# Kernel tuning notes

Measured on AMD Instinct MI355X. Metric: run time of the kernel, lower is better.

The kernel has to match this reference:

```python
import jax, jax.numpy as jnp
import numpy as np

BN_EPS = 1e-5


def _gin_layer(x, agg, W1, b1, W2, b2, gamma, beta):
    # GINConv with eps=0: h = MLP(x + sum_{j in N(i)} x_j)
    h = x + agg
    h = jax.nn.relu(h @ W1 + b1)
    h = jax.nn.relu(h @ W2 + b2)
    # BatchNorm1d, training mode (batch statistics, biased variance)
    mean = jnp.mean(h, axis=0)
    var = jnp.var(h, axis=0)
    return (h - mean) * jax.lax.rsqrt(var + BN_EPS) * gamma + beta


def setup_inputs() -> dict:
    key = jax.random.key(0)
    ks = jax.random.split(key, 10)
    N, E, D_IN, D_H, D_OUT = 100000, 1600000, 128, 128, 128
    s = lambda fi, fo: (2.0 / (fi + fo)) ** 0.5
    return {
        "x": jax.random.normal(ks[0], (N, D_IN), dtype=jnp.float32),
        "edge_index": jax.random.randint(ks[1], (2, E), 0, N, dtype=jnp.int64),
        "W1a": jax.random.normal(ks[2], (D_IN, D_H), dtype=jnp.float32) * s(D_IN, D_H),
        "b1a": jnp.zeros((D_H,), jnp.float32),
        "W1b": jax.random.normal(ks[3], (D_H, D_H), dtype=jnp.float32) * s(D_H, D_H),
        "b1b": jnp.zeros((D_H,), jnp.float32),
        "g1": jnp.ones((D_H,), jnp.float32),
        "be1": jnp.zeros((D_H,), jnp.float32),
        "W2a": jax.random.normal(ks[4], (D_H, D_H), dtype=jnp.float32) * s(D_H, D_H),
        "b2a": jnp.zeros((D_H,), jnp.float32),
        "W2b": jax.random.normal(ks[5], (D_H, D_OUT), dtype=jnp.float32) * s(D_H, D_OUT),
        "b2b": jnp.zeros((D_OUT,), jnp.float32),
        "g2": jnp.ones((D_OUT,), jnp.float32),
        "be2": jnp.zeros((D_OUT,), jnp.float32),
    }


def reference(x, edge_index, W1a, b1a, W1b, b1b, g1, be1,
              W2a, b2a, W2b, b2b, g2, be2):
    N = x.shape[0]
    src, dst = edge_index[0], edge_index[1]
    # layer 1: scatter-add neighbor features into targets
    agg = jax.ops.segment_sum(x[src], dst, num_segments=N)
    h = _gin_layer(x, agg, W1a, b1a, W1b, b1b, g1, be1)
    # layer 2
    agg = jax.ops.segment_sum(h[src], dst, num_segments=N)
    h = _gin_layer(h, agg, W2a, b2a, W2b, b2b, g2, be2)
    return h
```

## Files before the change

kernel.cpp:

```cpp
#include <hip/hip_runtime.h>
#include <hip/hip_bf16.h>

typedef unsigned int u32;
typedef unsigned short u16;
typedef short bf16x8 __attribute__((ext_vector_type(8)));
typedef float f32x4 __attribute__((ext_vector_type(4)));

static __device__ __forceinline__ float bf_lo(u32 v) { return __uint_as_float(v << 16); }
static __device__ __forceinline__ float bf_hi(u32 v) { return __uint_as_float(v & 0xffff0000u); }
static __device__ __forceinline__ u16 f2bf(float f) {
    u32 u = __float_as_uint(f);
    u32 r = u + 0x7fffu + ((u >> 16) & 1u);
    return (u16)(r >> 16);
}
static __device__ __forceinline__ u32 pack2(float a, float b) {
    return ((u32)f2bf(b) << 16) | (u32)f2bf(a);
}

__global__ __launch_bounds__(256) void convert_k(const float* __restrict__ in,
                                                 u32* __restrict__ out2, int total4)
{
    for (int i = blockIdx.x * 256 + threadIdx.x; i < total4; i += gridDim.x * 256) {
        float4 v = reinterpret_cast<const float4*>(in)[i];
        out2[2 * i + 0] = pack2(v.x, v.y);
        out2[2 * i + 1] = pack2(v.z, v.w);
    }
}

__global__ __launch_bounds__(256) void wprep_k(const float* __restrict__ Wa,
                                               const float* __restrict__ Wb,
                                               const float* __restrict__ Wc,
                                               const float* __restrict__ Wd,
                                               u16* __restrict__ Wf)
{
    int g = blockIdx.x * 256 + threadIdx.x;
    int which = g >> 14;
    int t = g & 16383;
    const float* W = which == 0 ? Wa : which == 1 ? Wb : which == 2 ? Wc : Wd;
    int j  = t & 7;
    int l  = (t >> 3) & 63;
    int nb = (t >> 9) & 7;
    int kg = (t >> 12) & 3;
    int k  = kg * 32 + (l >> 4) * 8 + j;
    int n  = nb * 16 + (l & 15);
    Wf[g] = f2bf(W[k * 128 + n]);
}

__global__ __launch_bounds__(256) void bhist_k(const int* __restrict__ edst,
                                               int* __restrict__ gcount, int E, int NB)
{
    __shared__ int lh[1024];
    for (int i = threadIdx.x; i < 1024; i += 256) lh[i] = 0;
    __syncthreads();
    for (int e = blockIdx.x * 256 + threadIdx.x; e < E; e += gridDim.x * 256)
        atomicAdd(&lh[edst[e] >> 7], 1);
    __syncthreads();
    for (int b = threadIdx.x; b < NB; b += 256)
        if (lh[b]) atomicAdd(&gcount[b], lh[b]);
}

__global__ __launch_bounds__(1024) void bscan_k(const int* __restrict__ gcount,
                                                int* __restrict__ goffs,
                                                int* __restrict__ gcur, int NB)
{
    __shared__ int s[1024];
    int t = threadIdx.x;
    int v = (t < NB) ? gcount[t] : 0;
    s[t] = v; __syncthreads();
    for (int d = 1; d < 1024; d <<= 1) {
        int x = (t >= d) ? s[t - d] : 0;
        __syncthreads();
        s[t] += x;
        __syncthreads();
    }
    if (t < NB) { int o = s[t] - v; goffs[t] = o; gcur[t] = o; }
    if (t == NB - 1) goffs[NB] = s[t];
}

__global__ __launch_bounds__(256) void bfill_k(const int* __restrict__ esrc,
                                               const int* __restrict__ edst,
                                               int* __restrict__ gcur,
                                               u32* __restrict__ bpacked, int E, int NB)
{
    __shared__ int lh[1024];
    __shared__ int lbase[1024];
    int t = threadIdx.x;
    for (int i = t; i < 1024; i += 256) lh[i] = 0;
    __syncthreads();
    int per = (E + gridDim.x - 1) / gridDim.x;
    int lo = blockIdx.x * per;
    int hi = lo + per; if (hi > E) hi = E;
    for (int e = lo + t; e < hi; e += 256) atomicAdd(&lh[edst[e] >> 7], 1);
    __syncthreads();
    for (int b = t; b < NB; b += 256) {
        int c = lh[b];
        lbase[b] = c ? atomicAdd(&gcur[b], c) : 0;
    }
    __syncthreads();
    for (int i = t; i < 1024; i += 256) lh[i] = 0;
    __syncthreads();
    for (int e = lo + t; e < hi; e += 256) {
        int d = edst[e];
        int b = d >> 7;
        int idx = atomicAdd(&lh[b], 1);
        bpacked[lbase[b] + idx] = ((u32)(d & 127) << 17) | (u32)esrc[e];
    }
}

__global__ __launch_bounds__(256) void fsort_k(const u32* __restrict__ bpacked,
                                               const int* __restrict__ goffs,
                                               int* __restrict__ slots,
                                               int* __restrict__ offs,
                                               int* __restrict__ deg, int N)
{
    __shared__ int cnt[128];
    __shared__ int roff[128];
    __shared__ int sb[128];
    int b = blockIdx.x, t = threadIdx.x;
    int start = goffs[b], end = goffs[b + 1];
    if (t < 128) cnt[t] = 0;
    __syncthreads();
    for (int e = start + t; e < end; e += 256)
        atomicAdd(&cnt[bpacked[e] >> 17], 1);
    __syncthreads();
    if (t < 128) sb[t] = cnt[t];
    __syncthreads();
    for (int d = 1; d < 128; d <<= 1) {
        int x = (t < 128 && t >= d) ? sb[t - d] : 0;
        __syncthreads();
        if (t < 128) sb[t] += x;
        __syncthreads();
    }
    if (t < 128) roff[t] = sb[t] - cnt[t];
    __syncthreads();
    int row0 = b * 128;
    if (t < 128 && row0 + t < N) {
        offs[row0 + t] = start + roff[t];
        deg[row0 + t]  = cnt[t];
    }
    if (t < 128) cnt[t] = 0;
    __syncthreads();
    for (int e = start + t; e < end; e += 256) {
        u32 pk = bpacked[e];
        int local = (int)(pk >> 17);
        int idx = atomicAdd(&cnt[local], 1);
        slots[start + roff[local] + idx] = (int)(pk & 0x1FFFF);
    }
}

#define ROWP(s) reinterpret_cast<const u32*>(xbase + ((size_t)(u32)(s) << 8))

template<int MODE>
__global__ __launch_bounds__(256) void gather_k(const u32* __restrict__ xb2,
                                                const int* __restrict__ offs,
                                                const int* __restrict__ deg,
                                                const int* __restrict__ slots,
                                                const float* __restrict__ stats_in,
                                                const float* __restrict__ g_in,
                                                const float* __restrict__ be_in,
                                                u32* __restrict__ xa2, int N)
{
    __shared__ float sc[128], sh[128];
    int t = threadIdx.x;
    if (MODE == 1) {
        if (t < 128) {
            float invN = 1.0f / (float)N;
            float mean = stats_in[t] * invN;
            float var  = stats_in[128 + t] * invN - mean * mean;
            float s = g_in[t] * rsqrtf(var + 1e-5f);
            sc[t] = s;
            sh[t] = be_in[t] - mean * s;
        }
        __syncthreads();
    }

    int row = blockIdx.x * 4 + (t >> 6);
    if (row >= N) return;
    int lane = t & 63;
    const char* xbase = (const char*)xb2;

    u32 self = ROWP(row)[lane];
    float ax0 = bf_lo(self), ay0 = bf_hi(self);
    float ax1 = 0.f, ay1 = 0.f, ax2 = 0.f, ay2 = 0.f, ax3 = 0.f, ay3 = 0.f;

    int ustart = __builtin_amdgcn_readfirstlane(offs[row]);
    int udg    = __builtin_amdgcn_readfirstlane(deg[row]);

    int e = 0;
    for (; e + 16 <= udg; e += 16) {
        int s0 = slots[ustart + e + 0],  s1 = slots[ustart + e + 1];
        int s2 = slots[ustart + e + 2],  s3 = slots[ustart + e + 3];
        int s4 = slots[ustart + e + 4],  s5 = slots[ustart + e + 5];
        int s6 = slots[ustart + e + 6],  s7 = slots[ustart + e + 7];
        int s8 = slots[ustart + e + 8],  s9 = slots[ustart + e + 9];
        int sA = slots[ustart + e + 10], sB = slots[ustart + e + 11];
        int sC = slots[ustart + e + 12], sD = slots[ustart + e + 13];
        int sE = slots[ustart + e + 14], sF = slots[ustart + e + 15];
        u32 v0 = ROWP(s0)[lane], v1 = ROWP(s1)[lane];
        u32 v2 = ROWP(s2)[lane], v3 = ROWP(s3)[lane];
        u32 v4 = ROWP(s4)[lane], v5 = ROWP(s5)[lane];
        u32 v6 = ROWP(s6)[lane], v7 = ROWP(s7)[lane];
        u32 v8 = ROWP(s8)[lane], v9 = ROWP(s9)[lane];
        u32 vA = ROWP(sA)[lane], vB = ROWP(sB)[lane];
        u32 vC = ROWP(sC)[lane], vD = ROWP(sD)[lane];
        u32 vE = ROWP(sE)[lane], vF = ROWP(sF)[lane];
        ax0 += bf_lo(v0); ay0 += bf_hi(v0);  ax1 += bf_lo(v1); ay1 += bf_hi(v1);
        ax2 += bf_lo(v2); ay2 += bf_hi(v2);  ax3 += bf_lo(v3); ay3 += bf_hi(v3);
        ax0 += bf_lo(v4); ay0 += bf_hi(v4);  ax1 += bf_lo(v5); ay1 += bf_hi(v5);
        ax2 += bf_lo(v6); ay2 += bf_hi(v6);  ax3 += bf_lo(v7); ay3 += bf_hi(v7);
        ax0 += bf_lo(v8); ay0 += bf_hi(v8);  ax1 += bf_lo(v9); ay1 += bf_hi(v9);
        ax2 += bf_lo(vA); ay2 += bf_hi(vA);  ax3 += bf_lo(vB); ay3 += bf_hi(vB);
        ax0 += bf_lo(vC); ay0 += bf_hi(vC);  ax1 += bf_lo(vD); ay1 += bf_hi(vD);
        ax2 += bf_lo(vE); ay2 += bf_hi(vE);  ax3 += bf_lo(vF); ay3 += bf_hi(vF);
    }
    if (e + 8 <= udg) {
        int s0 = slots[ustart + e + 0], s1 = slots[ustart + e + 1];
        int s2 = slots[ustart + e + 2], s3 = slots[ustart + e + 3];
        int s4 = slots[ustart + e + 4], s5 = slots[ustart + e + 5];
        int s6 = slots[ustart + e + 6], s7 = slots[ustart + e + 7];
        u32 v0 = ROWP(s0)[lane], v1 = ROWP(s1)[lane];
        u32 v2 = ROWP(s2)[lane], v3 = ROWP(s3)[lane];
        u32 v4 = ROWP(s4)[lane], v5 = ROWP(s5)[lane];
        u32 v6 = ROWP(s6)[lane], v7 = ROWP(s7)[lane];
        ax0 += bf_lo(v0); ay0 += bf_hi(v0);  ax1 += bf_lo(v1); ay1 += bf_hi(v1);
        ax2 += bf_lo(v2); ay2 += bf_hi(v2);  ax3 += bf_lo(v3); ay3 += bf_hi(v3);
        ax0 += bf_lo(v4); ay0 += bf_hi(v4);  ax1 += bf_lo(v5); ay1 += bf_hi(v5);
        ax2 += bf_lo(v6); ay2 += bf_hi(v6);  ax3 += bf_lo(v7); ay3 += bf_hi(v7);
        e += 8;
    }
    if (e + 4 <= udg) {
        int s0 = slots[ustart + e + 0], s1 = slots[ustart + e + 1];
        int s2 = slots[ustart + e + 2], s3 = slots[ustart + e + 3];
        u32 v0 = ROWP(s0)[lane], v1 = ROWP(s1)[lane];
        u32 v2 = ROWP(s2)[lane], v3 = ROWP(s3)[lane];
        ax0 += bf_lo(v0); ay0 += bf_hi(v0);  ax1 += bf_lo(v1); ay1 += bf_hi(v1);
        ax2 += bf_lo(v2); ay2 += bf_hi(v2);  ax3 += bf_lo(v3); ay3 += bf_hi(v3);
        e += 4;
    }
    for (; e < udg; ++e) {
        int s = slots[ustart + e];
        u32 v = ROWP(s)[lane];
        ax0 += bf_lo(v); ay0 += bf_hi(v);
    }

    float ax = (ax0 + ax1) + (ax2 + ax3);
    float ay = (ay0 + ay1) + (ay2 + ay3);
    if (MODE == 1) {
        float d1 = (float)(udg + 1);
        ax = sc[2 * lane]     * ax + d1 * sh[2 * lane];
        ay = sc[2 * lane + 1] * ay + d1 * sh[2 * lane + 1];
    }
    xa2[(size_t)row * 64 + lane] = pack2(ax, ay);
}

__global__ __launch_bounds__(256) void mlp_mfma_k(
    const u16* __restrict__ xa,
    const u16* __restrict__ wfa, const float* __restrict__ ba,
    const u16* __restrict__ wfb, const float* __restrict__ bb,
    u16* __restrict__ hb_out, float* __restrict__ partial, int N)
{
    __shared__ short ta[64 * 128];
    __shared__ float ssum[256];

    int t = threadIdx.x;
    int w = t >> 6, l = t & 63;
    int row0 = blockIdx.x * 64;

    for (int c = t; c < 1024; c += 256) {
        int r = c >> 4, ci = c & 15;
        int dst = (r * 128 + ci * 8) ^ ((r & 7) << 3);
        f32x4 v;
        if (row0 + r < N)
            v = *reinterpret_cast<const f32x4*>(xa + ((size_t)(row0 + r) * 128 + ci * 8));
        else
            v = f32x4{0.f, 0.f, 0.f, 0.f};
        *reinterpret_cast<f32x4*>(ta + dst) = v;
    }

    bf16x8 wf[2][4];
#pragma unroll
    for (int nr = 0; nr < 2; ++nr) {
        int nb = 2 * w + nr;
#pragma unroll
        for (int kg = 0; kg < 4; ++kg)
            wf[nr][kg] = *reinterpret_cast<const bf16x8*>(
                wfa + ((size_t)((kg * 8 + nb) * 64 + l)) * 8);
    }
    __syncthreads();

    int rr = l & 15;
    int kg8 = l >> 4;

    f32x4 acc[4][2];
#pragma unroll
    for (int mr = 0; mr < 4; ++mr)
#pragma unroll
        for (int nr = 0; nr < 2; ++nr)
            acc[mr][nr] = f32x4{0.f, 0.f, 0.f, 0.f};

#pragma unroll
    for (int mr = 0; mr < 4; ++mr) {
        int r = mr * 16 + rr;
        bf16x8 af[4];
#pragma unroll
        for (int kg = 0; kg < 4; ++kg) {
            int idx = (r * 128 + kg * 32 + kg8 * 8) ^ ((r & 7) << 3);
            af[kg] = *reinterpret_cast<const bf16x8*>(ta + idx);
        }
#pragma unroll
        for (int nr = 0; nr < 2; ++nr)
#pragma unroll
            for (int kg = 0; kg < 4; ++kg)
                acc[mr][nr] = __builtin_amdgcn_mfma_f32_16x16x32_bf16(
                    af[kg], wf[nr][kg], acc[mr][nr], 0, 0, 0);
    }
    __syncthreads();

    int colb = w * 32;
    float b0 = ba[colb + rr];
    float b1 = ba[colb + 16 + rr];
#pragma unroll
    for (int mr = 0; mr < 4; ++mr)
#pragma unroll
        for (int nr = 0; nr < 2; ++nr) {
            float bb_ = nr ? b1 : b0;
            int col = colb + nr * 16 + rr;
#pragma unroll
            for (int reg = 0; reg < 4; ++reg) {
                int row = mr * 16 + kg8 * 4 + reg;
                float v = fmaxf(acc[mr][nr][reg] + bb_, 0.0f);
                ta[(row * 128 + col) ^ ((row & 7) << 3)] = (short)f2bf(v);
            }
        }

#pragma unroll
    for (int nr = 0; nr < 2; ++nr) {
        int nb = 2 * w + nr;
#pragma unroll
        for (int kg = 0; kg < 4; ++kg)
            wf[nr][kg] = *reinterpret_cast<const bf16x8*>(
                wfb + ((size_t)((kg * 8 + nb) * 64 + l)) * 8);
    }
    __syncthreads();

#pragma unroll
    for (int mr = 0; mr < 4; ++mr)
#pragma unroll
        for (int nr = 0; nr < 2; ++nr)
            acc[mr][nr] = f32x4{0.f, 0.f, 0.f, 0.f};

#pragma unroll
    for (int mr = 0; mr < 4; ++mr) {
        int r = mr * 16 + rr;
        bf16x8 af[4];
#pragma unroll
        for (int kg = 0; kg < 4; ++kg) {
            int idx = (r * 128 + kg * 32 + kg8 * 8) ^ ((r & 7) << 3);
            af[kg] = *reinterpret_cast<const bf16x8*>(ta + idx);
        }
#pragma unroll
        for (int nr = 0; nr < 2; ++nr)
#pragma unroll
            for (int kg = 0; kg < 4; ++kg)
                acc[mr][nr] = __builtin_amdgcn_mfma_f32_16x16x32_bf16(
                    af[kg], wf[nr][kg], acc[mr][nr], 0, 0, 0);
    }

    float c0 = bb[colb + rr];
    float c1 = bb[colb + 16 + rr];
    float s0 = 0.f, q0 = 0.f, s1 = 0.f, q1 = 0.f;
#pragma unroll
    for (int mr = 0; mr < 4; ++mr) {
#pragma unroll
        for (int reg = 0; reg < 4; ++reg) {
            int row = row0 + mr * 16 + kg8 * 4 + reg;
            bool ok = row < N;
            float v0 = fmaxf(acc[mr][0][reg] + c0, 0.0f);
            float v1 = fmaxf(acc[mr][1][reg] + c1, 0.0f);
            if (ok) {
                hb_out[(size_t)row * 128 + colb + rr]      = f2bf(v0);
                hb_out[(size_t)row * 128 + colb + 16 + rr] = f2bf(v1);
                s0 += v0; q0 += v0 * v0;
                s1 += v1; q1 += v1 * v1;
            }
        }
    }
    s0 += __shfl_xor(s0, 16); s0 += __shfl_xor(s0, 32);
    q0 += __shfl_xor(q0, 16); q0 += __shfl_xor(q0, 32);
    s1 += __shfl_xor(s1, 16); s1 += __shfl_xor(s1, 32);
    q1 += __shfl_xor(q1, 16); q1 += __shfl_xor(q1, 32);
    if (kg8 == 0) {
        ssum[colb + rr]            = s0;
        ssum[128 + colb + rr]      = q0;
        ssum[colb + 16 + rr]       = s1;
        ssum[128 + colb + 16 + rr] = q1;
    }
    __syncthreads();
    partial[(size_t)blockIdx.x * 256 + t] = ssum[t];
}

__global__ __launch_bounds__(256) void reduce_k(const float* __restrict__ partial,
                                                float* __restrict__ stats, int nrows)
{
    int t = threadIdx.x;
    int chunk = (nrows + gridDim.x - 1) / gridDim.x;
    int lo = blockIdx.x * chunk;
    int hi = lo + chunk; if (hi > nrows) hi = nrows;
    float acc = 0.f;
    for (int r = lo; r < hi; ++r)
        acc += partial[(size_t)r * 256 + t];
    if (hi > lo) atomicAdd(&stats[t], acc);
}

__global__ __launch_bounds__(256) void bn_apply_bf_k(
    const u32* __restrict__ h2b, const float* __restrict__ stats,
    const float* __restrict__ gamma, const float* __restrict__ beta,
    float* __restrict__ out, int N)
{
    __shared__ float sc[128], sh[128];
    int t = threadIdx.x;
    if (t < 128) {
        float invN = 1.0f / (float)N;
        float mean = stats[t] * invN;
        float var  = stats[128 + t] * invN - mean * mean;
        float s = gamma[t] * rsqrtf(var + 1e-5f);
        sc[t] = s;
        sh[t] = beta[t] - mean * s;
    }
    __syncthreads();
    int total2 = N * 64;
    for (int i = blockIdx.x * 256 + t; i < total2; i += gridDim.x * 256) {
        u32 v = h2b[i];
        int c = (i & 63) * 2;
        float2 o;
        o.x = bf_lo(v) * sc[c]     + sh[c];
        o.y = bf_hi(v) * sc[c + 1] + sh[c + 1];
        reinterpret_cast<float2*>(out)[i] = o;
    }
}

extern "C" void kernel_launch(void* const* d_in, const int* in_sizes, int n_in,
                              void* d_out, int out_size, void* d_ws, size_t ws_size,
                              hipStream_t stream)
{
    const float* x   = (const float*)d_in[0];
    const int*   ei  = (const int*)d_in[1];
    const float* W1a = (const float*)d_in[2];
    const float* b1a = (const float*)d_in[3];
    const float* W1b = (const float*)d_in[4];
    const float* b1b = (const float*)d_in[5];
    const float* g1  = (const float*)d_in[6];
    const float* be1 = (const float*)d_in[7];
    const float* W2a = (const float*)d_in[8];
    const float* b2a = (const float*)d_in[9];
    const float* W2b = (const float*)d_in[10];
    const float* b2b = (const float*)d_in[11];
    const float* g2  = (const float*)d_in[12];
    const float* be2 = (const float*)d_in[13];

    const int N = in_sizes[0] / 128;
    const int E = in_sizes[1] / 2;
    const int* esrc = ei;
    const int* edst = ei + E;
    const int NB = (N + 127) >> 7;

    const int mblocks = (N + 63) / 64;
    const int gblocks = (N + 3) / 4;

    char* p = (char*)d_ws;
    const size_t featb = (size_t)N * 128 * sizeof(u16);
    u16* xa = (u16*)p;            p += featb;
    u16* h1 = (u16*)p;            p += featb;
    u16* xb = (u16*)p;            p += featb;
    u16* wf = (u16*)p;            p += 4 * 16384 * sizeof(u16);
    int* slots = (int*)p;         p += (size_t)E * sizeof(int) + 64;
    int* deg   = (int*)p;         p += (size_t)N * sizeof(int);
    int* offs  = (int*)p;         p += (size_t)N * sizeof(int);
    int* gcount = (int*)p;        p += 1024 * sizeof(int);
    int* goffs  = (int*)p;        p += 1032 * sizeof(int);
    int* gcur   = (int*)p;        p += 1024 * sizeof(int);
    float* stats = (float*)p;     p += 512 * sizeof(float);
    float* partial = (float*)p;   p += (size_t)mblocks * 256 * sizeof(float);
    u32* bpacked = (u32*)xa;

    u16* wf1a = wf;
    u16* wf1b = wf + 16384;
    u16* wf2a = wf + 32768;
    u16* wf2b = wf + 49152;
    float* stats1 = stats;
    float* stats2 = stats + 256;

    float* h = (float*)d_out;

    hipMemsetAsync(gcount, 0, 1024 * sizeof(int), stream);
    bhist_k<<<256, 256, 0, stream>>>(edst, gcount, E, NB);
    bscan_k<<<1, 1024, 0, stream>>>(gcount, goffs, gcur, NB);
    bfill_k<<<256, 256, 0, stream>>>(esrc, edst, gcur, bpacked, E, NB);
    fsort_k<<<NB, 256, 0, stream>>>(bpacked, goffs, slots, offs, deg, N);
    convert_k<<<2048, 256, 0, stream>>>(x, (u32*)xb, N * 32);
    wprep_k<<<256, 256, 0, stream>>>(W1a, W1b, W2a, W2b, wf);
    hipMemsetAsync(stats, 0, 512 * sizeof(float), stream);

    gather_k<0><<<gblocks, 256, 0, stream>>>((const u32*)xb, offs, deg, slots,
                                             nullptr, nullptr, nullptr, (u32*)xa, N);
    mlp_mfma_k<<<mblocks, 256, 0, stream>>>(xa, wf1a, b1a, wf1b, b1b,
                                            h1, partial, N);
    reduce_k<<<32, 256, 0, stream>>>(partial, stats1, mblocks);

    gather_k<1><<<gblocks, 256, 0, stream>>>((const u32*)h1, offs, deg, slots,
                                             stats1, g1, be1, (u32*)xa, N);
    mlp_mfma_k<<<mblocks, 256, 0, stream>>>(xa, wf2a, b2a, wf2b, b2b,
                                            h1, partial, N);
    reduce_k<<<32, 256, 0, stream>>>(partial, stats2, mblocks);

    bn_apply_bf_k<<<2048, 256, 0, stream>>>((const u32*)h1, stats2, g2, be2, h, N);
}
```

Baseline: 281.9 us.

## Fuse prep kernels, predicate gather tail, prefetch second-layer weights early

Merges the input conversion, destination histogram and weight-packing kernels into one launch split by block index, removing two launches. Replaces the gather's 8/4/1 remainder cascade with a single predicated block of up to 15 loads so the tail's loads can be issued together. In the MLP kernel, the second weight fragments are loaded into separate registers before the first epilogue so their latency overlaps the LDS writes. This adds register pressure, and the tail reads slot indices past the row end, which could run past the slots buffer on the last row.

```diff
diff --git a/kernel.cpp b/kernel.cpp
--- a/kernel.cpp
+++ b/kernel.cpp
@@ -17,46 +17,45 @@
     return ((u32)f2bf(b) << 16) | (u32)f2bf(a);
 }
 
-__global__ __launch_bounds__(256) void convert_k(const float* __restrict__ in,
-                                                 u32* __restrict__ out2, int total4)
-{
-    for (int i = blockIdx.x * 256 + threadIdx.x; i < total4; i += gridDim.x * 256) {
-        float4 v = reinterpret_cast<const float4*>(in)[i];
-        out2[2 * i + 0] = pack2(v.x, v.y);
-        out2[2 * i + 1] = pack2(v.z, v.w);
-    }
-}
-
-__global__ __launch_bounds__(256) void wprep_k(const float* __restrict__ Wa,
-                                               const float* __restrict__ Wb,
-                                               const float* __restrict__ Wc,
-                                               const float* __restrict__ Wd,
-                                               u16* __restrict__ Wf)
-{
-    int g = blockIdx.x * 256 + threadIdx.x;
-    int which = g >> 14;
-    int t = g & 16383;
-    const float* W = which == 0 ? Wa : which == 1 ? Wb : which == 2 ? Wc : Wd;
-    int j  = t & 7;
-    int l  = (t >> 3) & 63;
-    int nb = (t >> 9) & 7;
-    int kg = (t >> 12) & 3;
-    int k  = kg * 32 + (l >> 4) * 8 + j;
-    int n  = nb * 16 + (l & 15);
-    Wf[g] = f2bf(W[k * 128 + n]);
-}
-
-__global__ __launch_bounds__(256) void bhist_k(const int* __restrict__ edst,
-                                               int* __restrict__ gcount, int E, int NB)
-{
-    __shared__ int lh[1024];
-    for (int i = threadIdx.x; i < 1024; i += 256) lh[i] = 0;
-    __syncthreads();
-    for (int e = blockIdx.x * 256 + threadIdx.x; e < E; e += gridDim.x * 256)
-        atomicAdd(&lh[edst[e] >> 7], 1);
-    __syncthreads();
-    for (int b = threadIdx.x; b < NB; b += 256)
-        if (lh[b]) atomicAdd(&gcount[b], lh[b]);
+__global__ __launch_bounds__(256) void prep_k(const float* __restrict__ x,
+                                              u32* __restrict__ out2, int total4,
+                                              const int* __restrict__ edst,
+                                              int* __restrict__ gcount, int E, int NB,
+                                              const float* __restrict__ Wa,
+                                              const float* __restrict__ Wb,
+                                              const float* __restrict__ Wc,
+                                              const float* __restrict__ Wd,
+                                              u16* __restrict__ Wf)
+{
+    int b = blockIdx.x, t = threadIdx.x;
+    if (b < 2048) {
+        for (int i = b * 256 + t; i < total4; i += 2048 * 256) {
+            float4 v = reinterpret_cast<const float4*>(x)[i];
+            out2[2 * i + 0] = pack2(v.x, v.y);
+            out2[2 * i + 1] = pack2(v.z, v.w);
+        }
+    } else if (b < 2304) {
+        __shared__ int lh[1024];
+        for (int i = t; i < 1024; i += 256) lh[i] = 0;
+        __syncthreads();
+        for (int e = (b - 2048) * 256 + t; e < E; e += 256 * 256)
+            atomicAdd(&lh[edst[e] >> 7], 1);
+        __syncthreads();
+        for (int bb = t; bb < NB; bb += 256)
+            if (lh[bb]) atomicAdd(&gcount[bb], lh[bb]);
+    } else {
+        int g = (b - 2304) * 256 + t;
+        int which = g >> 14;
+        int tt = g & 16383;
+        const float* W = which == 0 ? Wa : which == 1 ? Wb : which == 2 ? Wc : Wd;
+        int j  = tt & 7;
+        int l  = (tt >> 3) & 63;
+        int nb = (tt >> 9) & 7;
+        int kg = (tt >> 12) & 3;
+        int k  = kg * 32 + (l >> 4) * 8 + j;
+        int n  = nb * 16 + (l & 15);
+        Wf[g] = f2bf(W[k * 128 + n]);
+    }
 }
 
 __global__ __launch_bounds__(1024) void bscan_k(const int* __restrict__ gcount,
@@ -213,34 +212,41 @@
         ax0 += bf_lo(vC); ay0 += bf_hi(vC);  ax1 += bf_lo(vD); ay1 += bf_hi(vD);
         ax2 += bf_lo(vE); ay2 += bf_hi(vE);  ax3 += bf_lo(vF); ay3 += bf_hi(vF);
     }
-    if (e + 8 <= udg) {
-        int s0 = slots[ustart + e + 0], s1 = slots[ustart + e + 1];
-        int s2 = slots[ustart + e + 2], s3 = slots[ustart + e + 3];
-        int s4 = slots[ustart + e + 4], s5 = slots[ustart + e + 5];
-        int s6 = slots[ustart + e + 6], s7 = slots[ustart + e + 7];
-        u32 v0 = ROWP(s0)[lane], v1 = ROWP(s1)[lane];
-        u32 v2 = ROWP(s2)[lane], v3 = ROWP(s3)[lane];
-        u32 v4 = ROWP(s4)[lane], v5 = ROWP(s5)[lane];
-        u32 v6 = ROWP(s6)[lane], v7 = ROWP(s7)[lane];
+    int k = udg - e;
+    if (k) {
+        int s0 = slots[ustart + e + 0],  s1 = slots[ustart + e + 1];
+        int s2 = slots[ustart + e + 2],  s3 = slots[ustart + e + 3];
+        int s4 = slots[ustart + e + 4],  s5 = slots[ustart + e + 5];
+        int s6 = slots[ustart + e + 6],  s7 = slots[ustart + e + 7];
+        int s8 = slots[ustart + e + 8],  s9 = slots[ustart + e + 9];
+        int sA = slots[ustart + e + 10], sB = slots[ustart + e + 11];
+        int sC = slots[ustart + e + 12], sD = slots[ustart + e + 13];
+        int sE = slots[ustart + e + 14];
+        u32 v0 = 0, v1 = 0, v2 = 0, v3 = 0, v4 = 0, v5 = 0, v6 = 0, v7 = 0;
+        u32 v8 = 0, v9 = 0, vA = 0, vB = 0, vC = 0, vD = 0, vE = 0;
+        v0 = ROWP(s0)[lane];
+        if (k > 1)  v1 = ROWP(s1)[lane];
+        if (k > 2)  v2 = ROWP(s2)[lane];
+        if (k > 3)  v3 = ROWP(s3)[lane];
+        if (k > 4)  v4 = ROWP(s4)[lane];
+        if (k > 5)  v5 = ROWP(s5)[lane];
+        if (k > 6)  v6 = ROWP(s6)[lane];
+        if (k > 7)  v7 = ROWP(s7)[lane];
+        if (k > 8)  v8 = ROWP(s8)[lane];
+        if (k > 9)  v9 = ROWP(s9)[lane];
+        if (k > 10) vA = ROWP(sA)[lane];
+        if (k > 11) vB = ROWP(sB)[lane];
+        if (k > 12) vC = ROWP(sC)[lane];
+        if (k > 13) vD = ROWP(sD)[lane];
+        if (k > 14) vE = ROWP(sE)[lane];
         ax0 += bf_lo(v0); ay0 += bf_hi(v0);  ax1 += bf_lo(v1); ay1 += bf_hi(v1);
         ax2 += bf_lo(v2); ay2 += bf_hi(v2);  ax3 += bf_lo(v3); ay3 += bf_hi(v3);
         ax0 += bf_lo(v4); ay0 += bf_hi(v4);  ax1 += bf_lo(v5); ay1 += bf_hi(v5);
         ax2 += bf_lo(v6); ay2 += bf_hi(v6);  ax3 += bf_lo(v7); ay3 += bf_hi(v7);
-        e += 8;
-    }
-    if (e + 4 <= udg) {
-        int s0 = slots[ustart + e + 0], s1 = slots[ustart + e + 1];
-        int s2 = slots[ustart + e + 2], s3 = slots[ustart + e + 3];
-        u32 v0 = ROWP(s0)[lane], v1 = ROWP(s1)[lane];
-        u32 v2 = ROWP(s2)[lane], v3 = ROWP(s3)[lane];
-        ax0 += bf_lo(v0); ay0 += bf_hi(v0);  ax1 += bf_lo(v1); ay1 += bf_hi(v1);
-        ax2 += bf_lo(v2); ay2 += bf_hi(v2);  ax3 += bf_lo(v3); ay3 += bf_hi(v3);
-        e += 4;
-    }
-    for (; e < udg; ++e) {
-        int s = slots[ustart + e];
-        u32 v = ROWP(s)[lane];
-        ax0 += bf_lo(v); ay0 += bf_hi(v);
+        ax0 += bf_lo(v8); ay0 += bf_hi(v8);  ax1 += bf_lo(v9); ay1 += bf_hi(v9);
+        ax2 += bf_lo(vA); ay2 += bf_hi(vA);  ax3 += bf_lo(vB); ay3 += bf_hi(vB);
+        ax0 += bf_lo(vC); ay0 += bf_hi(vC);  ax1 += bf_lo(vD); ay1 += bf_hi(vD);
+        ax2 += bf_lo(vE); ay2 += bf_hi(vE);
     }
 
     float ax = (ax0 + ax1) + (ax2 + ax3);
@@ -316,6 +322,16 @@
     }
     __syncthreads();
 
+    bf16x8 wf2[2][4];
+#pragma unroll
+    for (int nr = 0; nr < 2; ++nr) {
+        int nb = 2 * w + nr;
+#pragma unroll
+        for (int kg = 0; kg < 4; ++kg)
+            wf2[nr][kg] = *reinterpret_cast<const bf16x8*>(
+                wfb + ((size_t)((kg * 8 + nb) * 64 + l)) * 8);
+    }
+
     int colb = w * 32;
     float b0 = ba[colb + rr];
     float b1 = ba[colb + 16 + rr];
@@ -332,15 +348,6 @@
                 ta[(row * 128 + col) ^ ((row & 7) << 3)] = (short)f2bf(v);
             }
         }
-
-#pragma unroll
-    for (int nr = 0; nr < 2; ++nr) {
-        int nb = 2 * w + nr;
-#pragma unroll
-        for (int kg = 0; kg < 4; ++kg)
-            wf[nr][kg] = *reinterpret_cast<const bf16x8*>(
-                wfb + ((size_t)((kg * 8 + nb) * 64 + l)) * 8);
-    }
     __syncthreads();
 
 #pragma unroll
@@ -363,7 +370,7 @@
 #pragma unroll
             for (int kg = 0; kg < 4; ++kg)
                 acc[mr][nr] = __builtin_amdgcn_mfma_f32_16x16x32_bf16(
-                    af[kg], wf[nr][kg], acc[mr][nr], 0, 0, 0);
+                    af[kg], wf2[nr][kg], acc[mr][nr], 0, 0, 0);
     }
 
     float c0 = bb[colb + rr];
@@ -493,12 +500,12 @@
     float* h = (float*)d_out;
 
     hipMemsetAsync(gcount, 0, 1024 * sizeof(int), stream);
-    bhist_k<<<256, 256, 0, stream>>>(edst, gcount, E, NB);
+    prep_k<<<2560, 256, 0, stream>>>(x, (u32*)xb, N * 32,
+                                     edst, gcount, E, NB,
+                                     W1a, W1b, W2a, W2b, wf);
     bscan_k<<<1, 1024, 0, stream>>>(gcount, goffs, gcur, NB);
     bfill_k<<<256, 256, 0, stream>>>(esrc, edst, gcur, bpacked, E, NB);
     fsort_k<<<NB, 256, 0, stream>>>(bpacked, goffs, slots, offs, deg, N);
-    convert_k<<<2048, 256, 0, stream>>>(x, (u32*)xb, N * 32);
-    wprep_k<<<256, 256, 0, stream>>>(W1a, W1b, W2a, W2b, wf);
     hipMemsetAsync(stats, 0, 512 * sizeof(float), stream);
 
     gather_k<0><<<gblocks, 256, 0, stream>>>((const u32*)xb, offs, deg, slots,
```

Result: faster. 275.4 us (-2.3%).
